# Kernel tuning notes

Measured on AMD Instinct MI355X. Metric: run time of the kernel, lower is better.

## Reference

```python
import jax, jax.numpy as jnp
import numpy as np

N_NODES = 500_000
N_EDGES = 8_000_000


def setup_inputs() -> dict:
    key = jax.random.key(0)
    ks = jax.random.split(key, 10)
    x = jax.random.normal(ks[0], (N_NODES, 34), dtype=jnp.float32)
    edge_index = jax.random.randint(ks[1], (2, N_EDGES), 0, N_NODES, dtype=jnp.int32)

    def w(k, fan_in, fan_out):
        s = 1.0 / np.sqrt(fan_in)
        return jax.random.uniform(k, (fan_in, fan_out), jnp.float32, -s, s)

    return {
        "x": x,
        "edge_index": edge_index,
        "W1": w(ks[2], 34, 4), "b1": jnp.zeros((4,), jnp.float32),
        "W2": w(ks[3], 4, 4),  "b2": jnp.zeros((4,), jnp.float32),
        "W3": w(ks[4], 4, 2),  "b3": jnp.zeros((2,), jnp.float32),
        "Wl": w(ks[5], 2, 4),  "bl": jax.random.uniform(ks[6], (4,), jnp.float32, -0.7, 0.7),
    }


def reference(x, edge_index, W1, b1, W2, b2, W3, b3, Wl, bl):
    n = x.shape[0]
    # GCNConv: add self loops, symmetric normalization D^-1/2 (A+I) D^-1/2
    loops = jnp.arange(n, dtype=edge_index.dtype)
    src = jnp.concatenate([edge_index[0], loops])  # [E+N]
    dst = jnp.concatenate([edge_index[1], loops])  # [E+N]
    deg = jax.ops.segment_sum(jnp.ones_like(dst, jnp.float32), dst, num_segments=n)
    dinv = jnp.where(deg > 0, jax.lax.rsqrt(deg), 0.0)  # deg >= 1 with self loops
    norm = (dinv[src] * dinv[dst])[:, None]  # [E+N, 1]

    def gcn(h, W, b):
        h = h @ W                                   # [N, F_out] transform first
        msg = h[src] * norm                         # gather + scale per edge
        return jax.ops.segment_sum(msg, dst, num_segments=n) + b

    h = jax.nn.relu(gcn(x, W1, b1))
    h = jax.nn.relu(gcn(h, W2, b2))
    h = jax.nn.relu(gcn(h, W3, b3))   # [N, 2] -- returned as second output
    out = h @ Wl + bl                 # [N, 4]; original's out.relu() is not in-place, so no relu
    return out, h
```

## Files before the change

### kernel.cpp

```cpp
#include <hip/hip_runtime.h>
#include <hip/hip_fp16.h>
#include <hip/hip_cooperative_groups.h>

namespace cg = cooperative_groups;


#define MAXBUK 1024
#define BUCKET_BITS 9
#define BUCKET 512
#define PAD 16
#define REGION 9216

#define BIN_BLK 512
#define BIN_CHUNK 16384

#define SB_BLK 512
#define STAGE_MAX REGION

#define AGG_BLK 256
#define SMAX_A 4864

typedef unsigned u32;
typedef int      v4i __attribute__((ext_vector_type(4)));
typedef unsigned v4u __attribute__((ext_vector_type(4)));
typedef float    v2f __attribute__((ext_vector_type(2)));
typedef float    v4f __attribute__((ext_vector_type(4)));

__device__ __forceinline__ u32 ntl_u32(const u32* p) { return __builtin_nontemporal_load(p); }
__device__ __forceinline__ v4i ntl_v4i(const v4i* p) { return __builtin_nontemporal_load(p); }
__device__ __forceinline__ v4u ntl_v4u(const v4u* p) { return __builtin_nontemporal_load(p); }

__device__ __forceinline__ void unp4(uint2 pk, float& x0, float& x1, float& x2, float& x3) {
    __half2 lo = *(__half2*)&pk.x;
    __half2 hi = *(__half2*)&pk.y;
    float2 a = __half22float2(lo);
    float2 c = __half22float2(hi);
    x0 = a.x; x1 = a.y; x2 = c.x; x3 = c.y;
}

__global__ void init_kernel(int* __restrict__ gcur, int nbuk) {
    int i = blockIdx.x * 256 + threadIdx.x;
    if (i < nbuk) gcur[i * PAD] = i * REGION;
}

__global__ void __launch_bounds__(BIN_BLK, 1)
bin_kernel(const int* __restrict__ src, const int* __restrict__ dst,
           int* __restrict__ gcur, unsigned* __restrict__ ep, int E, int nbuk) {
    __shared__ int hist[MAXBUK];
    __shared__ int lbase[MAXBUK + 1];
    __shared__ int gb[MAXBUK];
    __shared__ int stmp[BIN_BLK];
    __shared__ int scarry;
    __shared__ unsigned stage[BIN_CHUNK];
    int t = threadIdx.x;
    for (int b = t; b < nbuk; b += BIN_BLK) hist[b] = 0;
    if (t == 0) scarry = 0;
    __syncthreads();
    int e0 = blockIdx.x * BIN_CHUNK;
    int e1 = min(e0 + BIN_CHUNK, E);
    int cn = e1 - e0;
    const v4i* dv = (const v4i*)(dst + e0);
    const v4i* sv = (const v4i*)(src + e0);
    int n4 = cn >> 2;
    for (int i = t; i < n4; i += BIN_BLK) {
        v4i d = dv[i];
        atomicAdd(&hist[d.x >> BUCKET_BITS], 1);
        atomicAdd(&hist[d.y >> BUCKET_BITS], 1);
        atomicAdd(&hist[d.z >> BUCKET_BITS], 1);
        atomicAdd(&hist[d.w >> BUCKET_BITS], 1);
    }
    for (int e = (n4 << 2) + t; e < cn; e += BIN_BLK)
        atomicAdd(&hist[dst[e0 + e] >> BUCKET_BITS], 1);
    __syncthreads();
    for (int base = 0; base < nbuk; base += BIN_BLK) {
        int i = base + t;
        int v = (i < nbuk) ? hist[i] : 0;
        stmp[t] = v;
        __syncthreads();
        for (int off = 1; off < BIN_BLK; off <<= 1) {
            int add = (t >= off) ? stmp[t - off] : 0;
            __syncthreads();
            stmp[t] += add;
            __syncthreads();
        }
        if (i < nbuk) lbase[i] = stmp[t] - v + scarry;
        __syncthreads();
        if (t == BIN_BLK - 1) scarry += stmp[t];
        __syncthreads();
    }
    if (t == 0) lbase[nbuk] = scarry;
    for (int b = t; b < nbuk; b += BIN_BLK) {
        int c = hist[b];
        gb[b] = c ? atomicAdd(&gcur[b * PAD], c) : 0;
        hist[b] = 0;
    }
    __syncthreads();
    for (int i = t; i < n4; i += BIN_BLK) {
        v4i d = ntl_v4i(dv + i);
        v4i s = ntl_v4i(sv + i);
        int bk, r;
        bk = d.x >> BUCKET_BITS; r = atomicAdd(&hist[bk], 1);
        stage[lbase[bk] + r] = ((unsigned)(d.x & (BUCKET - 1)) << 23) | (unsigned)s.x;
        bk = d.y >> BUCKET_BITS; r = atomicAdd(&hist[bk], 1);
        stage[lbase[bk] + r] = ((unsigned)(d.y & (BUCKET - 1)) << 23) | (unsigned)s.y;
        bk = d.z >> BUCKET_BITS; r = atomicAdd(&hist[bk], 1);
        stage[lbase[bk] + r] = ((unsigned)(d.z & (BUCKET - 1)) << 23) | (unsigned)s.z;
        bk = d.w >> BUCKET_BITS; r = atomicAdd(&hist[bk], 1);
        stage[lbase[bk] + r] = ((unsigned)(d.w & (BUCKET - 1)) << 23) | (unsigned)s.w;
    }
    for (int e = (n4 << 2) + t; e < cn; e += BIN_BLK) {
        int d = dst[e0 + e];
        int bk = d >> BUCKET_BITS;
        int r = atomicAdd(&hist[bk], 1);
        stage[lbase[bk] + r] = ((unsigned)(d & (BUCKET - 1)) << 23) | (unsigned)src[e0 + e];
    }
    __syncthreads();
    int wid = t >> 6, lane = t & 63;
    for (int b = wid; b < nbuk; b += (BIN_BLK >> 6)) {
        int lo = lbase[b];
        int c = lbase[b + 1] - lo;
        unsigned* dp = ep + gb[b];
        for (int j = lane; j < c; j += 64)
            __builtin_nontemporal_store(stage[lo + j], dp + j);
    }
}

__global__ void __launch_bounds__(SB_BLK)
sortb_kernel(unsigned* __restrict__ ep, const int* __restrict__ gcur,
             const float* __restrict__ x, const float* __restrict__ W1,
             float* __restrict__ dinv, int* __restrict__ nodeoff,
             int* __restrict__ bend, uint2* __restrict__ g1h, int N, int nbuk) {
    __shared__ __align__(16) unsigned stage[STAGE_MAX];
    __shared__ int cnt[BUCKET];
    __shared__ int wsum[8];
    __shared__ float sW[136];
    int t = threadIdx.x, b = blockIdx.x;
    if (t < 136) sW[t] = W1[t];
    cnt[t] = 0;
    int ps = b * REGION;
    int cn = min(gcur[b * PAD] - ps, STAGE_MAX);
    const v4u* epv = (const v4u*)(ep + ps);
    int n4 = cn >> 2;
    for (int j = t; j < n4; j += SB_BLK) ((v4u*)stage)[j] = ntl_v4u(epv + j);
    for (int j = (n4 << 2) + t; j < cn; j += SB_BLK) stage[j] = ntl_u32(ep + ps + j);
    if (t == 0) bend[b] = ps + cn;
    __syncthreads();
    for (int j = t; j < cn; j += SB_BLK) atomicAdd(&cnt[stage[j] >> 23], 1);
    __syncthreads();
    int deg = cnt[t];
    int v = deg;
#pragma unroll
    for (int off = 1; off < 64; off <<= 1) {
        int n = __shfl_up(v, off);
        if ((t & 63) >= off) v += n;
    }
    if ((t & 63) == 63) wsum[t >> 6] = v;
    __syncthreads();
    if (t == 0) {
        int run = 0;
#pragma unroll
        for (int w = 0; w < 8; ++w) { int c = wsum[w]; wsum[w] = run; run += c; }
    }
    __syncthreads();
    int excl = v + wsum[t >> 6] - deg;
    int gbase = b << BUCKET_BITS;
    int nn = min(BUCKET, N - gbase);
    if (t < nn) nodeoff[gbase + t] = ps + excl;
    cnt[t] = excl;
    __syncthreads();
    for (int j = t; j < cn; j += SB_BLK) {
        unsigned u = stage[j];
        int r = atomicAdd(&cnt[u >> 23], 1);
        ep[ps + r] = u & 0x7FFFFFu;
    }
    int i = gbase + t;
    if (t < nn) {
        float dv = rsqrtf((float)deg + 1.0f);
        dinv[i] = dv;
        const v2f* xr = (const v2f*)(x + (size_t)i * 34);
        float o0 = 0.f, o1 = 0.f, o2 = 0.f, o3 = 0.f;
#pragma unroll
        for (int k = 0; k < 17; ++k) {
            v2f vv = __builtin_nontemporal_load(xr + k);
            o0 = fmaf(vv.x, sW[(2 * k) * 4 + 0], o0);
            o1 = fmaf(vv.x, sW[(2 * k) * 4 + 1], o1);
            o2 = fmaf(vv.x, sW[(2 * k) * 4 + 2], o2);
            o3 = fmaf(vv.x, sW[(2 * k) * 4 + 3], o3);
            o0 = fmaf(vv.y, sW[(2 * k + 1) * 4 + 0], o0);
            o1 = fmaf(vv.y, sW[(2 * k + 1) * 4 + 1], o1);
            o2 = fmaf(vv.y, sW[(2 * k + 1) * 4 + 2], o2);
            o3 = fmaf(vv.y, sW[(2 * k + 1) * 4 + 3], o3);
        }
        __half2 lo = __floats2half2_rn(o0 * dv, o1 * dv);
        __half2 hi = __floats2half2_rn(o2 * dv, o3 * dv);
        uint2 pk;
        pk.x = *(unsigned*)&lo;
        pk.y = *(unsigned*)&hi;
        g1h[i] = pk;
    }
}

__device__ __forceinline__ void phase1(int i, int lo, int hi, int cs, int s,
        const unsigned* se, const unsigned* __restrict__ esrc,
        const uint2* __restrict__ g1h, float dv,
        const float* __restrict__ b1, const float* __restrict__ W2,
        uint2* __restrict__ g2h) {
    float a0, a1, a2, a3;
    unp4(g1h[i], a0, a1, a2, a3);
    int hi2 = min(hi, cs);
    int j = lo;
    for (; j + 4 <= hi2; j += 4) {
        unsigned s0 = se[j], s1 = se[j + 1], s2 = se[j + 2], s3 = se[j + 3];
        uint2 q0 = g1h[s0], q1 = g1h[s1], q2 = g1h[s2], q3 = g1h[s3];
        float t0, t1, t2, t3;
        unp4(q0, t0, t1, t2, t3); a0 += t0; a1 += t1; a2 += t2; a3 += t3;
        unp4(q1, t0, t1, t2, t3); a0 += t0; a1 += t1; a2 += t2; a3 += t3;
        unp4(q2, t0, t1, t2, t3); a0 += t0; a1 += t1; a2 += t2; a3 += t3;
        unp4(q3, t0, t1, t2, t3); a0 += t0; a1 += t1; a2 += t2; a3 += t3;
    }
    for (; j < hi2; ++j) {
        float t0, t1, t2, t3;
        unp4(g1h[se[j]], t0, t1, t2, t3);
        a0 += t0; a1 += t1; a2 += t2; a3 += t3;
    }
    for (; j < hi; ++j) {
        float t0, t1, t2, t3;
        unp4(g1h[ntl_u32(esrc + s + j)], t0, t1, t2, t3);
        a0 += t0; a1 += t1; a2 += t2; a3 += t3;
    }
    float h0 = fmaxf(fmaf(a0, dv, b1[0]), 0.f);
    float h1 = fmaxf(fmaf(a1, dv, b1[1]), 0.f);
    float h2 = fmaxf(fmaf(a2, dv, b1[2]), 0.f);
    float h3 = fmaxf(fmaf(a3, dv, b1[3]), 0.f);
    float o0 = dv * (h0 * W2[0] + h1 * W2[4] + h2 * W2[8] + h3 * W2[12]);
    float o1 = dv * (h0 * W2[1] + h1 * W2[5] + h2 * W2[9] + h3 * W2[13]);
    float o2 = dv * (h0 * W2[2] + h1 * W2[6] + h2 * W2[10] + h3 * W2[14]);
    float o3 = dv * (h0 * W2[3] + h1 * W2[7] + h2 * W2[11] + h3 * W2[15]);
    __half2 lo2 = __floats2half2_rn(o0, o1);
    __half2 hi3 = __floats2half2_rn(o2, o3);
    uint2 pk;
    pk.x = *(unsigned*)&lo2;
    pk.y = *(unsigned*)&hi3;
    g2h[i] = pk;
}

__device__ __forceinline__ void phase2(int i, int lo, int hi, int cs, int s,
        const unsigned* se, const unsigned* __restrict__ esrc,
        const uint2* __restrict__ g2h, float dv,
        const float* __restrict__ b2, const float* __restrict__ W3,
        unsigned* __restrict__ g3h) {
    float a0, a1, a2, a3;
    unp4(g2h[i], a0, a1, a2, a3);
    int hi2 = min(hi, cs);
    int j = lo;
    for (; j + 4 <= hi2; j += 4) {
        unsigned s0 = se[j], s1 = se[j + 1], s2 = se[j + 2], s3 = se[j + 3];
        uint2 q0 = g2h[s0], q1 = g2h[s1], q2 = g2h[s2], q3 = g2h[s3];
        float t0, t1, t2, t3;
        unp4(q0, t0, t1, t2, t3); a0 += t0; a1 += t1; a2 += t2; a3 += t3;
        unp4(q1, t0, t1, t2, t3); a0 += t0; a1 += t1; a2 += t2; a3 += t3;
        unp4(q2, t0, t1, t2, t3); a0 += t0; a1 += t1; a2 += t2; a3 += t3;
        unp4(q3, t0, t1, t2, t3); a0 += t0; a1 += t1; a2 += t2; a3 += t3;
    }
    for (; j < hi2; ++j) {
        float t0, t1, t2, t3;
        unp4(g2h[se[j]], t0, t1, t2, t3);
        a0 += t0; a1 += t1; a2 += t2; a3 += t3;
    }
    for (; j < hi; ++j) {
        float t0, t1, t2, t3;
        unp4(g2h[ntl_u32(esrc + s + j)], t0, t1, t2, t3);
        a0 += t0; a1 += t1; a2 += t2; a3 += t3;
    }
    float h0 = fmaxf(fmaf(a0, dv, b2[0]), 0.f);
    float h1 = fmaxf(fmaf(a1, dv, b2[1]), 0.f);
    float h2 = fmaxf(fmaf(a2, dv, b2[2]), 0.f);
    float h3 = fmaxf(fmaf(a3, dv, b2[3]), 0.f);
    float o0 = dv * (h0 * W3[0] + h1 * W3[2] + h2 * W3[4] + h3 * W3[6]);
    float o1 = dv * (h0 * W3[1] + h1 * W3[3] + h2 * W3[5] + h3 * W3[7]);
    __half2 oo = __floats2half2_rn(o0, o1);
    g3h[i] = *(unsigned*)&oo;
}

__device__ __forceinline__ void phase3(int i, int lo, int hi, int cs, int s,
        const unsigned* se, const unsigned* __restrict__ esrc,
        const unsigned* __restrict__ g3h, float dv,
        const float* __restrict__ b3, const float* __restrict__ Wl,
        const float* __restrict__ bl, float* __restrict__ out, int N) {
    unsigned pk = g3h[i];
    float2 v = __half22float2(*(__half2*)&pk);
    float ax = v.x, ay = v.y;
    int hi2 = min(hi, cs);
    int j = lo;
    for (; j + 4 <= hi2; j += 4) {
        unsigned q0 = g3h[se[j]], q1 = g3h[se[j + 1]];
        unsigned q2 = g3h[se[j + 2]], q3 = g3h[se[j + 3]];
        float2 v0 = __half22float2(*(__half2*)&q0);
        float2 v1 = __half22float2(*(__half2*)&q1);
        float2 v2 = __half22float2(*(__half2*)&q2);
        float2 v3 = __half22float2(*(__half2*)&q3);
        ax += v0.x + v1.x + v2.x + v3.x;
        ay += v0.y + v1.y + v2.y + v3.y;
    }
    for (; j < hi2; ++j) {
        unsigned q = g3h[se[j]];
        float2 w = __half22float2(*(__half2*)&q);
        ax += w.x; ay += w.y;
    }
    for (; j < hi; ++j) {
        unsigned q = g3h[ntl_u32(esrc + s + j)];
        float2 w = __half22float2(*(__half2*)&q);
        ax += w.x; ay += w.y;
    }
    float h0 = fmaxf(fmaf(ax, dv, b3[0]), 0.f);
    float h1 = fmaxf(fmaf(ay, dv, b3[1]), 0.f);
    v4f oo;
    oo.x = fmaf(h0, Wl[0], fmaf(h1, Wl[4], bl[0]));
    oo.y = fmaf(h0, Wl[1], fmaf(h1, Wl[5], bl[1]));
    oo.z = fmaf(h0, Wl[2], fmaf(h1, Wl[6], bl[2]));
    oo.w = fmaf(h0, Wl[3], fmaf(h1, Wl[7], bl[3]));
    __builtin_nontemporal_store(oo, (v4f*)out + i);
    v2f h; h.x = h0; h.y = h1;
    __builtin_nontemporal_store(h, (v2f*)(out + (size_t)4 * N) + i);
}

struct BlkGeo { int s, cs, lo, hi; bool act; int i; float dv; };

__device__ __forceinline__ BlkGeo geo(const int* __restrict__ nodeoff,
                                      const int* __restrict__ bend,
                                      const float* __restrict__ dinv, int N) {
    BlkGeo g;
    int t = threadIdx.x, blk = blockIdx.x, buk = blk >> 1;
    int gbase = (buk << BUCKET_BITS) + ((blk & 1) << 8);
    int nn = min(256, N - gbase);
    g.i = gbase + t;
    g.act = (nn > 0) && (t < nn);
    g.s = 0; g.cs = 0; g.lo = 0; g.hi = 0; g.dv = 0.f;
    if (nn > 0) {
        g.s = nodeoff[gbase];
        int nbn = min(512, N - (buk << BUCKET_BITS));
        bool lasthalf = (blk & 1) ? true : (nbn <= 256);
        int e = lasthalf ? bend[buk] : nodeoff[gbase + 256];
        g.cs = min(e - g.s, SMAX_A);
        if (g.act) {
            bool lastnode = lasthalf && (t == nn - 1);
            g.lo = nodeoff[g.i] - g.s;
            g.hi = (lastnode ? bend[buk] : nodeoff[g.i + 1]) - g.s;
            g.dv = dinv[g.i];
        }
    }
    return g;
}

__global__ void __launch_bounds__(AGG_BLK, 8)
aggf_kernel(const unsigned* __restrict__ esrc, const int* __restrict__ nodeoff,
            const int* __restrict__ bend, const float* __restrict__ dinv,
            uint2* __restrict__ g1h, uint2* __restrict__ g2h,
            const float* __restrict__ b1, const float* __restrict__ W2,
            const float* __restrict__ b2, const float* __restrict__ W3,
            const float* __restrict__ b3, const float* __restrict__ Wl,
            const float* __restrict__ bl, float* __restrict__ out, int N) {
    cg::grid_group gg = cg::this_grid();
    __shared__ unsigned se[SMAX_A];
    BlkGeo g = geo(nodeoff, bend, dinv, N);
    int t = threadIdx.x;
    for (int j = t; j < g.cs; j += AGG_BLK) se[j] = ntl_u32(esrc + g.s + j);
    __syncthreads();
    if (g.act) phase1(g.i, g.lo, g.hi, g.cs, g.s, se, esrc, g1h, g.dv, b1, W2, g2h);
    gg.sync();
    unsigned* g3h = (unsigned*)g1h;
    if (g.act) phase2(g.i, g.lo, g.hi, g.cs, g.s, se, esrc, g2h, g.dv, b2, W3, g3h);
    gg.sync();
    if (g.act) phase3(g.i, g.lo, g.hi, g.cs, g.s, se, esrc, g3h, g.dv, b3, Wl, bl, out, N);
}

template <int P>
__global__ void __launch_bounds__(AGG_BLK)
aggp_kernel(const unsigned* __restrict__ esrc, const int* __restrict__ nodeoff,
            const int* __restrict__ bend, const float* __restrict__ dinv,
            uint2* __restrict__ g1h, uint2* __restrict__ g2h,
            const float* __restrict__ b1, const float* __restrict__ W2,
            const float* __restrict__ b2, const float* __restrict__ W3,
            const float* __restrict__ b3, const float* __restrict__ Wl,
            const float* __restrict__ bl, float* __restrict__ out, int N) {
    __shared__ unsigned se[SMAX_A];
    BlkGeo g = geo(nodeoff, bend, dinv, N);
    int t = threadIdx.x;
    for (int j = t; j < g.cs; j += AGG_BLK) se[j] = ntl_u32(esrc + g.s + j);
    __syncthreads();
    unsigned* g3h = (unsigned*)g1h;
    if (g.act) {
        if (P == 1) phase1(g.i, g.lo, g.hi, g.cs, g.s, se, esrc, g1h, g.dv, b1, W2, g2h);
        if (P == 2) phase2(g.i, g.lo, g.hi, g.cs, g.s, se, esrc, g2h, g.dv, b2, W3, g3h);
        if (P == 3) phase3(g.i, g.lo, g.hi, g.cs, g.s, se, esrc, g3h, g.dv, b3, Wl, bl, out, N);
    }
}

extern "C" void kernel_launch(void* const* d_in, const int* in_sizes, int n_in,
                              void* d_out, int out_size, void* d_ws, size_t ws_size,
                              hipStream_t stream) {
    const float* x  = (const float*)d_in[0];
    const int*   ei = (const int*)d_in[1];
    const float* W1 = (const float*)d_in[2];
    const float* b1 = (const float*)d_in[3];
    const float* W2 = (const float*)d_in[4];
    const float* b2 = (const float*)d_in[5];
    const float* W3 = (const float*)d_in[6];
    const float* b3 = (const float*)d_in[7];
    const float* Wl = (const float*)d_in[8];
    const float* bl = (const float*)d_in[9];
    float* out = (float*)d_out;

    int N = in_sizes[0] / 34;
    const int E = in_sizes[1] / 2;
    const int* src = ei;
    const int* dst = ei + E;
    const int NBUK = (N + BUCKET - 1) >> BUCKET_BITS;

    auto al16 = [](size_t v) { return (v + 15) & ~(size_t)15; };
    char* w = (char*)d_ws;
    size_t off = 0;
    int*      gcur    = (int*)(w + off);      off += al16((size_t)NBUK * PAD * 4);
    int*      bend    = (int*)(w + off);      off += al16((size_t)NBUK * 4);
    float*    dinv    = (float*)(w + off);    off += al16((size_t)N * 4);
    int*      nodeoff = (int*)(w + off);      off += al16((size_t)(N + 1) * 4);
    unsigned* ep      = (unsigned*)(w + off); off += al16((size_t)NBUK * REGION * 4);
    uint2*    g1h     = (uint2*)(w + off);    off += al16((size_t)(N + 1) * 8);
    uint2*    g2h     = (uint2*)(w + off);

    const int nb_bin = (E + BIN_CHUNK - 1) / BIN_CHUNK;
    const int nb_agg = 2 * NBUK;

    init_kernel<<<(NBUK + 255) / 256, 256, 0, stream>>>(gcur, NBUK);
    bin_kernel<<<nb_bin, BIN_BLK, 0, stream>>>(src, dst, gcur, ep, E, NBUK);
    sortb_kernel<<<NBUK, SB_BLK, 0, stream>>>(ep, gcur, x, W1, dinv, nodeoff, bend, g1h, N, NBUK);

    int blocksPerCU = 0, ncu = 0, dev = 0;
    hipGetDevice(&dev);
    hipDeviceGetAttribute(&ncu, hipDeviceAttributeMultiprocessorCount, dev);
    hipOccupancyMaxActiveBlocksPerMultiprocessor(&blocksPerCU, (const void*)aggf_kernel, AGG_BLK, 0);
    if (blocksPerCU * ncu >= nb_agg) {
        void* args[] = {(void*)&ep, (void*)&nodeoff, (void*)&bend, (void*)&dinv,
                        (void*)&g1h, (void*)&g2h, (void*)&b1, (void*)&W2,
                        (void*)&b2, (void*)&W3, (void*)&b3, (void*)&Wl,
                        (void*)&bl, (void*)&out, (void*)&N};
        hipLaunchCooperativeKernel((const void*)aggf_kernel, dim3(nb_agg), dim3(AGG_BLK),
                                   args, 0, stream);
    } else {
        aggp_kernel<1><<<nb_agg, AGG_BLK, 0, stream>>>(ep, nodeoff, bend, dinv, g1h, g2h,
                                                       b1, W2, b2, W3, b3, Wl, bl, out, N);
        aggp_kernel<2><<<nb_agg, AGG_BLK, 0, stream>>>(ep, nodeoff, bend, dinv, g1h, g2h,
                                                       b1, W2, b2, W3, b3, Wl, bl, out, N);
        aggp_kernel<3><<<nb_agg, AGG_BLK, 0, stream>>>(ep, nodeoff, bend, dinv, g1h, g2h,
                                                       b1, W2, b2, W3, b3, Wl, bl, out, N);
    }
}
```

Before: 291.9 us.

## Stage x rows through LDS, use wave-shuffle scan, unroll gathers by eight

The bin kernel's LDS Hillis-Steele scan, which needs many block barriers, is replaced by a wave-level shuffle scan plus a per-wave carry. The sort kernel now loads x rows into shared memory with coalesced 16-byte nontemporal loads before the 34-wide transform, instead of strided 8-byte per-thread row loads, and writes the sorted edge list with nontemporal stores. The three aggregation phases gain an 8-way unrolled gather loop so more loads are in flight. In exchange it adds extra barriers, reuses the stage and cnt LDS buffers, and increases register pressure in the gather loops.

```diff
diff --git a/kernel.cpp b/kernel.cpp
--- a/kernel.cpp
+++ b/kernel.cpp
@@ -29,6 +29,7 @@
 __device__ __forceinline__ u32 ntl_u32(const u32* p) { return __builtin_nontemporal_load(p); }
 __device__ __forceinline__ v4i ntl_v4i(const v4i* p) { return __builtin_nontemporal_load(p); }
 __device__ __forceinline__ v4u ntl_v4u(const v4u* p) { return __builtin_nontemporal_load(p); }
+__device__ __forceinline__ v4f ntl_v4f(const v4f* p) { return __builtin_nontemporal_load(p); }
 
 __device__ __forceinline__ void unp4(uint2 pk, float& x0, float& x1, float& x2, float& x3) {
     __half2 lo = *(__half2*)&pk.x;
@@ -49,7 +50,7 @@
     __shared__ int hist[MAXBUK];
     __shared__ int lbase[MAXBUK + 1];
     __shared__ int gb[MAXBUK];
-    __shared__ int stmp[BIN_BLK];
+    __shared__ int wsum2[8];
     __shared__ int scarry;
     __shared__ unsigned stage[BIN_CHUNK];
     int t = threadIdx.x;
@@ -75,17 +76,22 @@
     for (int base = 0; base < nbuk; base += BIN_BLK) {
         int i = base + t;
         int v = (i < nbuk) ? hist[i] : 0;
-        stmp[t] = v;
+        int sv2 = v;
+#pragma unroll
+        for (int off = 1; off < 64; off <<= 1) {
+            int n = __shfl_up(sv2, off);
+            if ((t & 63) >= off) sv2 += n;
+        }
+        if ((t & 63) == 63) wsum2[t >> 6] = sv2;
         __syncthreads();
-        for (int off = 1; off < BIN_BLK; off <<= 1) {
-            int add = (t >= off) ? stmp[t - off] : 0;
-            __syncthreads();
-            stmp[t] += add;
-            __syncthreads();
+        if (t == 0) {
+            int run = scarry;
+#pragma unroll
+            for (int w2 = 0; w2 < 8; ++w2) { int c = wsum2[w2]; wsum2[w2] = run; run += c; }
+            scarry = run;
         }
-        if (i < nbuk) lbase[i] = stmp[t] - v + scarry;
         __syncthreads();
-        if (t == BIN_BLK - 1) scarry += stmp[t];
+        if (i < nbuk) lbase[i] = sv2 - v + wsum2[t >> 6];
         __syncthreads();
     }
     if (t == 0) lbase[nbuk] = scarry;
@@ -148,6 +154,7 @@
     for (int j = t; j < cn; j += SB_BLK) atomicAdd(&cnt[stage[j] >> 23], 1);
     __syncthreads();
     int deg = cnt[t];
+    float dv = rsqrtf((float)deg + 1.0f);
     int v = deg;
 #pragma unroll
     for (int off = 1; off < 64; off <<= 1) {
@@ -165,40 +172,57 @@
     int excl = v + wsum[t >> 6] - deg;
     int gbase = b << BUCKET_BITS;
     int nn = min(BUCKET, N - gbase);
-    if (t < nn) nodeoff[gbase + t] = ps + excl;
+    if (t < nn) { nodeoff[gbase + t] = ps + excl; dinv[gbase + t] = dv; }
     cnt[t] = excl;
     __syncthreads();
     for (int j = t; j < cn; j += SB_BLK) {
         unsigned u = stage[j];
         int r = atomicAdd(&cnt[u >> 23], 1);
-        ep[ps + r] = u & 0x7FFFFFu;
-    }
-    int i = gbase + t;
-    if (t < nn) {
-        float dv = rsqrtf((float)deg + 1.0f);
-        dinv[i] = dv;
-        const v2f* xr = (const v2f*)(x + (size_t)i * 34);
-        float o0 = 0.f, o1 = 0.f, o2 = 0.f, o3 = 0.f;
+        __builtin_nontemporal_store(u & 0x7FFFFFu, ep + ps + r);
+    }
+    __syncthreads();
+    ((float*)cnt)[t] = dv;
+    float* xs = (float*)stage;
+    for (int hh = 0; hh < 2; ++hh) {
+        int rl = hh << 8;
+        int rows = nn - rl; rows = rows < 0 ? 0 : (rows > 256 ? 256 : rows);
+        if (rows > 0) {
+            if (hh == 1) __syncthreads();
+            int nfl = rows * 34;
+            const float* xsrc = x + (size_t)(gbase + rl) * 34;
+            int n4f = nfl >> 2;
+            for (int j = t; j < n4f; j += SB_BLK)
+                ((v4f*)xs)[j] = ntl_v4f((const v4f*)xsrc + j);
+            for (int j = (n4f << 2) + t; j < nfl; j += SB_BLK) xs[j] = xsrc[j];
+            __syncthreads();
+            if (t < rows) {
+                float dvv = ((float*)cnt)[rl + t];
+                const float* xr = xs + t * 34;
+                float o0 = 0.f, o1 = 0.f, o2 = 0.f, o3 = 0.f;
 #pragma unroll
-        for (int k = 0; k < 17; ++k) {
-            v2f vv = __builtin_nontemporal_load(xr + k);
-            o0 = fmaf(vv.x, sW[(2 * k) * 4 + 0], o0);
-            o1 = fmaf(vv.x, sW[(2 * k) * 4 + 1], o1);
-            o2 = fmaf(vv.x, sW[(2 * k) * 4 + 2], o2);
-            o3 = fmaf(vv.x, sW[(2 * k) * 4 + 3], o3);
-            o0 = fmaf(vv.y, sW[(2 * k + 1) * 4 + 0], o0);
-            o1 = fmaf(vv.y, sW[(2 * k + 1) * 4 + 1], o1);
-            o2 = fmaf(vv.y, sW[(2 * k + 1) * 4 + 2], o2);
-            o3 = fmaf(vv.y, sW[(2 * k + 1) * 4 + 3], o3);
+                for (int k = 0; k < 17; ++k) {
+                    float vx = xr[2 * k], vy = xr[2 * k + 1];
+                    o0 = fmaf(vx, sW[(2 * k) * 4 + 0], o0);
+                    o1 = fmaf(vx, sW[(2 * k) * 4 + 1], o1);
+                    o2 = fmaf(vx, sW[(2 * k) * 4 + 2], o2);
+                    o3 = fmaf(vx, sW[(2 * k) * 4 + 3], o3);
+                    o0 = fmaf(vy, sW[(2 * k + 1) * 4 + 0], o0);
+                    o1 = fmaf(vy, sW[(2 * k + 1) * 4 + 1], o1);
+                    o2 = fmaf(vy, sW[(2 * k + 1) * 4 + 2], o2);
+                    o3 = fmaf(vy, sW[(2 * k + 1) * 4 + 3], o3);
+                }
+                __half2 lo = __floats2half2_rn(o0 * dvv, o1 * dvv);
+                __half2 hi = __floats2half2_rn(o2 * dvv, o3 * dvv);
+                uint2 pk;
+                pk.x = *(unsigned*)&lo;
+                pk.y = *(unsigned*)&hi;
+                g1h[gbase + rl + t] = pk;
+            }
         }
-        __half2 lo = __floats2half2_rn(o0 * dv, o1 * dv);
-        __half2 hi = __floats2half2_rn(o2 * dv, o3 * dv);
-        uint2 pk;
-        pk.x = *(unsigned*)&lo;
-        pk.y = *(unsigned*)&hi;
-        g1h[i] = pk;
-    }
-}
+    }
+}
+
+#define ACC4(Q) { float t0,t1,t2,t3; unp4(Q,t0,t1,t2,t3); a0+=t0; a1+=t1; a2+=t2; a3+=t3; }
 
 __device__ __forceinline__ void phase1(int i, int lo, int hi, int cs, int s,
         const unsigned* se, const unsigned* __restrict__ esrc,
@@ -209,25 +233,20 @@
     unp4(g1h[i], a0, a1, a2, a3);
     int hi2 = min(hi, cs);
     int j = lo;
+    for (; j + 8 <= hi2; j += 8) {
+        unsigned s0 = se[j], s1 = se[j+1], s2 = se[j+2], s3 = se[j+3];
+        unsigned s4 = se[j+4], s5 = se[j+5], s6 = se[j+6], s7 = se[j+7];
+        uint2 q0 = g1h[s0], q1 = g1h[s1], q2 = g1h[s2], q3 = g1h[s3];
+        uint2 q4 = g1h[s4], q5 = g1h[s5], q6 = g1h[s6], q7 = g1h[s7];
+        ACC4(q0) ACC4(q1) ACC4(q2) ACC4(q3) ACC4(q4) ACC4(q5) ACC4(q6) ACC4(q7)
+    }
     for (; j + 4 <= hi2; j += 4) {
-        unsigned s0 = se[j], s1 = se[j + 1], s2 = se[j + 2], s3 = se[j + 3];
+        unsigned s0 = se[j], s1 = se[j+1], s2 = se[j+2], s3 = se[j+3];
         uint2 q0 = g1h[s0], q1 = g1h[s1], q2 = g1h[s2], q3 = g1h[s3];
-        float t0, t1, t2, t3;
-        unp4(q0, t0, t1, t2, t3); a0 += t0; a1 += t1; a2 += t2; a3 += t3;
-        unp4(q1, t0, t1, t2, t3); a0 += t0; a1 += t1; a2 += t2; a3 += t3;
-        unp4(q2, t0, t1, t2, t3); a0 += t0; a1 += t1; a2 += t2; a3 += t3;
-        unp4(q3, t0, t1, t2, t3); a0 += t0; a1 += t1; a2 += t2; a3 += t3;
-    }
-    for (; j < hi2; ++j) {
-        float t0, t1, t2, t3;
-        unp4(g1h[se[j]], t0, t1, t2, t3);
-        a0 += t0; a1 += t1; a2 += t2; a3 += t3;
-    }
-    for (; j < hi; ++j) {
-        float t0, t1, t2, t3;
-        unp4(g1h[ntl_u32(esrc + s + j)], t0, t1, t2, t3);
-        a0 += t0; a1 += t1; a2 += t2; a3 += t3;
-    }
+        ACC4(q0) ACC4(q1) ACC4(q2) ACC4(q3)
+    }
+    for (; j < hi2; ++j) ACC4(g1h[se[j]])
+    for (; j < hi; ++j) ACC4(g1h[ntl_u32(esrc + s + j)])
     float h0 = fmaxf(fmaf(a0, dv, b1[0]), 0.f);
     float h1 = fmaxf(fmaf(a1, dv, b1[1]), 0.f);
     float h2 = fmaxf(fmaf(a2, dv, b1[2]), 0.f);
@@ -253,25 +272,20 @@
     unp4(g2h[i], a0, a1, a2, a3);
     int hi2 = min(hi, cs);
     int j = lo;
+    for (; j + 8 <= hi2; j += 8) {
+        unsigned s0 = se[j], s1 = se[j+1], s2 = se[j+2], s3 = se[j+3];
+        unsigned s4 = se[j+4], s5 = se[j+5], s6 = se[j+6], s7 = se[j+7];
+        uint2 q0 = g2h[s0], q1 = g2h[s1], q2 = g2h[s2], q3 = g2h[s3];
+        uint2 q4 = g2h[s4], q5 = g2h[s5], q6 = g2h[s6], q7 = g2h[s7];
+        ACC4(q0) ACC4(q1) ACC4(q2) ACC4(q3) ACC4(q4) ACC4(q5) ACC4(q6) ACC4(q7)
+    }
     for (; j + 4 <= hi2; j += 4) {
-        unsigned s0 = se[j], s1 = se[j + 1], s2 = se[j + 2], s3 = se[j + 3];
+        unsigned s0 = se[j], s1 = se[j+1], s2 = se[j+2], s3 = se[j+3];
         uint2 q0 = g2h[s0], q1 = g2h[s1], q2 = g2h[s2], q3 = g2h[s3];
-        float t0, t1, t2, t3;
-        unp4(q0, t0, t1, t2, t3); a0 += t0; a1 += t1; a2 += t2; a3 += t3;
-        unp4(q1, t0, t1, t2, t3); a0 += t0; a1 += t1; a2 += t2; a3 += t3;
-        unp4(q2, t0, t1, t2, t3); a0 += t0; a1 += t1; a2 += t2; a3 += t3;
-        unp4(q3, t0, t1, t2, t3); a0 += t0; a1 += t1; a2 += t2; a3 += t3;
-    }
-    for (; j < hi2; ++j) {
-        float t0, t1, t2, t3;
-        unp4(g2h[se[j]], t0, t1, t2, t3);
-        a0 += t0; a1 += t1; a2 += t2; a3 += t3;
-    }
-    for (; j < hi; ++j) {
-        float t0, t1, t2, t3;
-        unp4(g2h[ntl_u32(esrc + s + j)], t0, t1, t2, t3);
-        a0 += t0; a1 += t1; a2 += t2; a3 += t3;
-    }
+        ACC4(q0) ACC4(q1) ACC4(q2) ACC4(q3)
+    }
+    for (; j < hi2; ++j) ACC4(g2h[se[j]])
+    for (; j < hi; ++j) ACC4(g2h[ntl_u32(esrc + s + j)])
     float h0 = fmaxf(fmaf(a0, dv, b2[0]), 0.f);
     float h1 = fmaxf(fmaf(a1, dv, b2[1]), 0.f);
     float h2 = fmaxf(fmaf(a2, dv, b2[2]), 0.f);
@@ -292,9 +306,22 @@
     float ax = v.x, ay = v.y;
     int hi2 = min(hi, cs);
     int j = lo;
+    for (; j + 8 <= hi2; j += 8) {
+        unsigned q0 = g3h[se[j]],   q1 = g3h[se[j+1]], q2 = g3h[se[j+2]], q3 = g3h[se[j+3]];
+        unsigned q4 = g3h[se[j+4]], q5 = g3h[se[j+5]], q6 = g3h[se[j+6]], q7 = g3h[se[j+7]];
+        float2 v0 = __half22float2(*(__half2*)&q0);
+        float2 v1 = __half22float2(*(__half2*)&q1);
+        float2 v2 = __half22float2(*(__half2*)&q2);
+        float2 v3 = __half22float2(*(__half2*)&q3);
+        float2 v4 = __half22float2(*(__half2*)&q4);
+        float2 v5 = __half22float2(*(__half2*)&q5);
+        float2 v6 = __half22float2(*(__half2*)&q6);
+        float2 v7 = __half22float2(*(__half2*)&q7);
+        ax += (v0.x + v1.x + v2.x + v3.x) + (v4.x + v5.x + v6.x + v7.x);
+        ay += (v0.y + v1.y + v2.y + v3.y) + (v4.y + v5.y + v6.y + v7.y);
+    }
     for (; j + 4 <= hi2; j += 4) {
-        unsigned q0 = g3h[se[j]], q1 = g3h[se[j + 1]];
-        unsigned q2 = g3h[se[j + 2]], q3 = g3h[se[j + 3]];
+        unsigned q0 = g3h[se[j]], q1 = g3h[se[j+1]], q2 = g3h[se[j+2]], q3 = g3h[se[j+3]];
         float2 v0 = __half22float2(*(__half2*)&q0);
         float2 v1 = __half22float2(*(__half2*)&q1);
         float2 v2 = __half22float2(*(__half2*)&q2);
```

After: 510.5 us. +74.9%, slower.
